# Kernel optimization log

Measured on AMD Instinct MI355X. Metric: run time of the kernel, lower is better.

## Reference

```python
import jax, jax.numpy as jnp
import numpy as np

N = 10000      # nodes
E = 160000     # edges
MUL = 64       # multiplicity of 0e and 1o in node feats / target
NATTR = 10     # number of element types (node_attrs one-hot width)
RDIM = 8       # radial (edge_feats) dim
NAVG = 16.0    # num_avg_neighbors
_INV3 = 0.5773502691896258  # CG coeff for 1o x 1o -> 0e (1/sqrt(3))


def setup_inputs() -> dict:
    key = jax.random.key(0)
    ks = jax.random.split(key, 20)
    return {
        "node_attrs": jax.random.uniform(ks[0], (N, NATTR), jnp.float32),
        "node_feats": jax.random.normal(ks[1], (N, 4 * MUL), jnp.float32),
        "edge_attrs_real": jax.random.normal(ks[2], (E, 4), jnp.float32),
        "edge_attrs_imag": jax.random.normal(ks[3], (E, 4), jnp.float32),
        "edge_feats": jax.random.normal(ks[4], (E, RDIM), jnp.float32),
        # linear_up (per-l internal weights)
        "W_up0": jax.random.normal(ks[5], (MUL, MUL), jnp.float32),
        "W_up1": jax.random.normal(ks[6], (MUL, MUL), jnp.float32),
        # conv_tp_weights MLP: [8, 64, 64, 64, 4*MUL]
        "M1": jax.random.normal(ks[7], (RDIM, 64), jnp.float32),
        "M2": jax.random.normal(ks[8], (64, 64), jnp.float32),
        "M3": jax.random.normal(ks[9], (64, 64), jnp.float32),
        "M4": jax.random.normal(ks[10], (64, 4 * MUL), jnp.float32),
        # linear: irreps_mid (128x0e+128x1o) -> irreps_nonlin (128x0e+64x1o)
        "W_lin_s": jax.random.normal(ks[11], (2 * MUL, 2 * MUL), jnp.float32),
        "W_lin_v": jax.random.normal(ks[12], (2 * MUL, MUL), jnp.float32),
        # skip_tp: FullyConnectedTensorProduct(node_feats, node_attrs -> irreps_nonlin)
        "W_sk_s": jax.random.normal(ks[13], (MUL, NATTR, 2 * MUL), jnp.float32),
        "W_sk_v": jax.random.normal(ks[14], (MUL, NATTR, MUL), jnp.float32),
        "edge_index": jax.random.randint(ks[15], (2, E), 0, N, jnp.int64
                                         if jax.config.jax_enable_x64 else jnp.int32),
    }


def _forward(node_attrs, node_feats, edge_attrs_real, edge_attrs_imag, edge_feats,
             W_up0, W_up1, M1, M2, M3, M4, W_lin_s, W_lin_v, W_sk_s, W_sk_v,
             sender, receiver):
    n = node_feats.shape[0]
    x0 = node_feats[:, :MUL]                          # (N, 64)   64x0e
    x1 = node_feats[:, MUL:].reshape(n, MUL, 3)       # (N, 64, 3) 64x1o

    # skip TP (fully connected, node_attrs are scalars)
    sk_norm = 1.0 / np.sqrt(MUL * NATTR)
    sc_s = jnp.einsum('nu,na,uav->nv', x0, node_attrs, W_sk_s) * sk_norm   # (N,128)
    sc_v = jnp.einsum('nui,na,uav->nvi', x1, node_attrs, W_sk_v) * sk_norm # (N,64,3)

    # linear_up (per-l)
    up_norm = 1.0 / np.sqrt(MUL)
    x0 = (x0 @ W_up0) * up_norm
    x1 = jnp.einsum('nui,uv->nvi', x1, W_up1) * up_norm

    # radial MLP -> per-edge TP weights (4 uvu paths x MUL)
    h = jax.nn.silu((edge_feats @ M1) / np.sqrt(RDIM))
    h = jax.nn.silu((h @ M2) / 8.0)
    h = jax.nn.silu((h @ M3) / 8.0)
    tw = (h @ M4) / 8.0                               # (E, 256)
    wA, wB, wC, wD = (tw[:, :MUL], tw[:, MUL:2*MUL],
                      tw[:, 2*MUL:3*MUL], tw[:, 3*MUL:])

    xs0 = x0[sender]                                  # (E, 64)
    xs1 = x1[sender]                                  # (E, 64, 3)

    def conv_tp(y):
        # y: (E,4) = [0e | 1o]; uvu paths with per-edge weights
        y0, y1 = y[:, :1], y[:, 1:]
        s = jnp.concatenate([xs0 * y0 * wA,                                  # 0e x 0e -> 0e
                             jnp.einsum('eui,ei->eu', xs1, y1) * _INV3 * wD  # 1o x 1o -> 0e
                             ], axis=1)                                      # (E,128)
        v = jnp.concatenate([(xs0 * wB)[:, :, None] * y1[:, None, :],        # 0e x 1o -> 1o
                             xs1 * (y0 * wC)[:, :, None]                     # 1o x 0e -> 1o
                             ], axis=1)                                      # (E,128,3)
        return s, v

    sr, vr = conv_tp(edge_attrs_real)
    si, vi = conv_tp(edge_attrs_imag)

    ms_r = jax.ops.segment_sum(sr, receiver, num_segments=n)
    mv_r = jax.ops.segment_sum(vr, receiver, num_segments=n)
    ms_i = jax.ops.segment_sum(si, receiver, num_segments=n)
    mv_i = jax.ops.segment_sum(vi, receiver, num_segments=n)

    lin_norm = (1.0 / np.sqrt(2 * MUL)) / (2.0 * NAVG)

    def lin(ms, mv):
        return (ms @ W_lin_s) * lin_norm, jnp.einsum('nui,uv->nvi', mv, W_lin_v) * lin_norm

    def gate(s, v):
        # irreps_nonlin = 64x0e scalars | 64x0e gates | 64x1o gated
        scal = jax.nn.silu(s[:, :MUL])
        g = jax.nn.silu(s[:, MUL:])
        return jnp.concatenate([scal, (v * g[:, :, None]).reshape(n, 3 * MUL)], axis=1)

    ls, lv = lin(ms_r, mv_r)
    real = gate(ls + sc_s, lv + sc_v)                 # (N, 256), residual on real part
    lsi, lvi = lin(ms_i, mv_i)
    imag = gate(lsi, lvi)                             # (N, 256)

    # view_as_complex + reshape [N, num_features, dim//num_features]; complex kept
    # as trailing real/imag axis of size 2.
    return jnp.stack([real, imag], axis=-1).reshape(n, MUL, (4 * MUL) // MUL, 2)


def reference(node_attrs, node_feats, edge_attrs_real, edge_attrs_imag, edge_feats,
              W_up0, W_up1, M1, M2, M3, M4, W_lin_s, W_lin_v, W_sk_s, W_sk_v,
              edge_index):
    sender, receiver = edge_index[0], edge_index[1]
    return _forward(node_attrs, node_feats, edge_attrs_real, edge_attrs_imag,
                    edge_feats, W_up0, W_up1, M1, M2, M3, M4,
                    W_lin_s, W_lin_v, W_sk_s, W_sk_v, sender, receiver)
```

## Files before the change

kernel.cpp:

```cpp
#include <hip/hip_runtime.h>
#include <hip/hip_bf16.h>

#define NN 10000
#define NE 160000
#define NGRP 625
#define XPLN 640000

#define SK_NORM   0.039528470752104741f
#define UP_NORM   0.125f
#define M1_NORM   0.35355339059327373f
#define INV3      0.5773502691896258f
#define LIN_NORM  0.0027621358640099516f

__device__ __forceinline__ float siluf(float x) { return x / (1.0f + __expf(-x)); }

__device__ __forceinline__ unsigned short f2bf_bits(float x) {
    union { __hip_bfloat16 h; unsigned short u; } cv;
    cv.h = __float2bfloat16(x);
    return cv.u;
}
__device__ __forceinline__ float bflo(unsigned int w) { return __uint_as_float(w << 16); }
__device__ __forceinline__ float bfhi(unsigned int w) { return __uint_as_float(w & 0xffff0000u); }

typedef short bf16x8 __attribute__((ext_vector_type(8)));
typedef float f32x4  __attribute__((ext_vector_type(4)));

__global__ __launch_bounds__(256) void k_detect(const int* __restrict__ ei32, int* __restrict__ flag) {
    __shared__ int cnt;
    if (threadIdx.x == 0) cnt = 0;
    __syncthreads();
    int z = 0;
    for (int i = threadIdx.x; i < 1024; i += 256)
        if (ei32[2 * i + 1] == 0) z++;
    atomicAdd(&cnt, z);
    __syncthreads();
    if (threadIdx.x == 0) flag[0] = (cnt >= 512) ? 1 : 0;
}

__global__ __launch_bounds__(256) void k_cvt(const int* __restrict__ ei32, const int* __restrict__ flag,
                                             int* __restrict__ snd, int* __restrict__ rcv) {
    int e = blockIdx.x * 256 + threadIdx.x;
    if (e >= NE) return;
    if (flag[0]) {
        const long long* e64 = (const long long*)ei32;
        snd[e] = (int)e64[e];
        rcv[e] = (int)e64[NE + e];
    } else {
        snd[e] = ei32[e];
        rcv[e] = ei32[NE + e];
    }
}

__global__ __launch_bounds__(256) void k_wprepN(
    const float* __restrict__ Wsk_s, const float* __restrict__ Wsk_v,
    const float* __restrict__ Wu0, const float* __restrict__ Wu1,
    unsigned short* __restrict__ WNF) {
    int idx = blockIdx.x * 256 + threadIdx.x;
    if (idx >= 131072) return;
    float val;
    if (idx < 81920) {
        int p = idx / 10240, r = idx % 10240;
        int kc = r >> 9, l8 = r & 511;
        int lane = l8 >> 3, j = l8 & 7, quad = lane >> 4, lo = lane & 15;
        int a = kc >> 1, u = (kc & 1) * 32 + quad * 8 + j;
        val = Wsk_s[(u * 10 + a) * 128 + p * 16 + lo];
    } else if (idx < 122880) {
        int rel = idx - 81920;
        int p = rel / 10240, r = rel % 10240;
        int kc = r >> 9, l8 = r & 511;
        int lane = l8 >> 3, j = l8 & 7, quad = lane >> 4, lo = lane & 15;
        int a = kc >> 1, u = (kc & 1) * 32 + quad * 8 + j;
        val = Wsk_v[(u * 10 + a) * 64 + p * 16 + lo];
    } else if (idx < 126976) {
        int rel = idx - 122880;
        int p = rel >> 10, r = rel & 1023;
        int kc = r >> 9, l8 = r & 511;
        int lane = l8 >> 3, j = l8 & 7, quad = lane >> 4, lo = lane & 15;
        int u = kc * 32 + quad * 8 + j;
        val = Wu0[u * 64 + p * 16 + lo];
    } else {
        int rel = idx - 126976;
        int p = rel >> 10, r = rel & 1023;
        int kc = r >> 9, l8 = r & 511;
        int lane = l8 >> 3, j = l8 & 7, quad = lane >> 4, lo = lane & 15;
        int u = kc * 32 + quad * 8 + j;
        val = Wu1[u * 64 + p * 16 + lo];
    }
    WNF[idx] = f2bf_bits(val);
}

__global__ __launch_bounds__(256) void k_xprep(
    const float* __restrict__ node_attrs, const float* __restrict__ node_feats,
    unsigned short* __restrict__ xpk, float* __restrict__ attrsP) {
    int idx = blockIdx.x * 256 + threadIdx.x;
    if (idx < 4 * NN * 64) {
        int n = idx >> 8, c = idx & 255;
        int plane = c >> 6, u = c & 63;
        float v = (plane == 0) ? node_feats[(long)n * 256 + u]
                               : node_feats[(long)n * 256 + 64 + u * 3 + (plane - 1)];
        xpk[(size_t)plane * XPLN + (long)n * 64 + u] = f2bf_bits(v);
        return;
    }
    int i2 = idx - 4 * NN * 64;
    if (i2 < 10 * NN) {
        int a = i2 / NN, n = i2 - a * NN;
        attrsP[i2] = node_attrs[(long)n * 10 + a];
    }
}

__global__ __launch_bounds__(256) void k_wprep2(
    const float* __restrict__ M1, const float* __restrict__ M2,
    const float* __restrict__ M3, const float* __restrict__ M4,
    const float* __restrict__ W_lin_s, const float* __restrict__ W_lin_v,
    unsigned short* __restrict__ WFG, unsigned short* __restrict__ WLF) {
    int idx = blockIdx.x * 256 + threadIdx.x;
    if (idx >= (52 + 48) * 512) return;
    if (idx < 52 * 512) {
        int f = idx >> 9, r = idx & 511;
        int lane = r >> 3, j = r & 7;
        int quad = lane >> 4, lo = lane & 15;
        float val;
        if (f < 4) {
            int n = f * 16 + lo, k = quad * 8 + j;
            val = (k < 8) ? M1[k * 64 + n] : 0.f;
        } else if (f < 12) {
            int g2 = f - 4, nt = g2 >> 1, half = g2 & 1;
            int n = nt * 16 + lo, k = half * 32 + quad * 8 + j;
            val = M2[k * 64 + n];
        } else if (f < 20) {
            int g3 = f - 12, nt = g3 >> 1, half = g3 & 1;
            int n = nt * 16 + lo, k = half * 32 + quad * 8 + j;
            val = M3[k * 64 + n];
        } else {
            int g4 = f - 20, tt = g4 >> 1, half = g4 & 1;
            int n = tt * 16 + lo, k = half * 32 + quad * 8 + j;
            val = M4[k * 256 + n];
        }
        WFG[idx] = f2bf_bits(val);
    } else {
        int rel = idx - 52 * 512;
        int f = rel >> 9, r = rel & 511;
        int lane = r >> 3, j = r & 7;
        int quad = lane >> 4, lo = lane & 15;
        float val;
        if (f < 32) {
            int vt = f >> 2, ks = f & 3;
            val = W_lin_s[(ks * 32 + quad * 8 + j) * 128 + vt * 16 + lo];
        } else {
            int f2 = f - 32;
            int vt = f2 >> 2, ks = f2 & 3;
            val = W_lin_v[(ks * 32 + quad * 8 + j) * 64 + vt * 16 + lo];
        }
        WLF[rel] = f2bf_bits(val);
    }
}

#define G0 8
#define NB0 79
#define G2 4
#define NB2 157
#define G3 16
#define NB3 40
#define KNODE_GRID (4*NB0 + 2*NB2 + 2*NB3)

__global__ __launch_bounds__(128) void k_node(
    const unsigned short* __restrict__ xpk, const float* __restrict__ attrsP,
    const unsigned short* __restrict__ WNF,
    float* __restrict__ sc_s, float* __restrict__ sc_v,
    float* __restrict__ x0u, float* __restrict__ x1p) {
    __shared__ unsigned short pan[2 * 10240];
    __shared__ float att[10 * 128];

    int t = threadIdx.x;
    int bid = blockIdx.x;
    int type, vp, chunk;
    if (bid < 4 * NB0)                 { type = 0; vp = bid / NB0; chunk = bid % NB0; }
    else if (bid < 4 * NB0 + 2 * NB2)  { int r = bid - 4 * NB0; type = 2; vp = r / NB2; chunk = r % NB2; }
    else                               { int r = bid - 4 * NB0 - 2 * NB2; type = 3; vp = r / NB3; chunk = r % NB3; }
    int G = (type == 0) ? G0 : (type == 2 ? G2 : G3);
    int g0 = chunk * G;
    int ng = NGRP - g0; if (ng > G) ng = G;
    int n0 = g0 * 16;

    int psrc, pcnt;
    if (type == 0)      { psrc = vp * 2 * 10240;           pcnt = 20480; }
    else if (type == 2) { psrc = 81920 + vp * 2 * 10240;   pcnt = 20480; }
    else                { psrc = 122880 + vp * 2 * 1024;   pcnt = 2048;  }
    for (int i = t; i < pcnt / 8; i += 128)
        ((float4*)pan)[i] = ((const float4*)(WNF + psrc))[i];
    if (type == 3) {
        for (int i = t; i < 2048 / 8; i += 128)
            ((float4*)(pan + 2048))[i] = ((const float4*)(WNF + 126976 + vp * 2 * 1024))[i];
    }
    if (type <= 2) {
        int cnt = ng * 16;
        #pragma unroll
        for (int k = 0; k < 10; k++) {
            int i = k * 128 + t;
            int nl = t;
            if (nl < cnt) att[i] = attrsP[k * NN + n0 + nl];
        }
    }
    __syncthreads();

    int wv = t >> 6, lane = t & 63, lo = lane & 15, quad = lane >> 4;
    int lbase = lane * 8;
    const f32x4 zacc = {0.f, 0.f, 0.f, 0.f};
    const unsigned short* mypan = pan + wv * 10240;

    if (type == 0) {
        int vtg = vp * 2 + wv;
        const unsigned short* xb = xpk;
        bf16x8 nfa0 = *(const bf16x8*)(xb + (long)(n0 + lo) * 64 + quad * 8);
        bf16x8 nfa1 = *(const bf16x8*)(xb + (long)(n0 + lo) * 64 + 32 + quad * 8);
        #pragma unroll 1
        for (int g = 0; g < ng; g++) {
            bf16x8 fa0 = nfa0, fa1 = nfa1;
            if (g + 1 < ng) {
                nfa0 = *(const bf16x8*)(xb + (long)(n0 + (g + 1) * 16 + lo) * 64 + quad * 8);
                nfa1 = *(const bf16x8*)(xb + (long)(n0 + (g + 1) * 16 + lo) * 64 + 32 + quad * 8);
            }
            f32x4 acc = zacc;
            #pragma unroll
            for (int a = 0; a < 10; a++) {
                bf16x8 b0 = *(const bf16x8*)&mypan[(2 * a) * 512 + lbase];
                bf16x8 b1 = *(const bf16x8*)&mypan[(2 * a + 1) * 512 + lbase];
                f32x4 p = __builtin_amdgcn_mfma_f32_16x16x32_bf16(fa0, b0, zacc, 0, 0, 0);
                p = __builtin_amdgcn_mfma_f32_16x16x32_bf16(fa1, b1, p, 0, 0, 0);
                float4 afv = *(const float4*)&att[a * 128 + g * 16 + quad * 4];
                acc[0] += afv.x * p[0]; acc[1] += afv.y * p[1];
                acc[2] += afv.z * p[2]; acc[3] += afv.w * p[3];
            }
            int nb = n0 + g * 16;
            #pragma unroll
            for (int r = 0; r < 4; r++)
                sc_s[(long)(nb + quad * 4 + r) * 128 + vtg * 16 + lo] = acc[r] * SK_NORM;
        }
    } else if (type == 2) {
        int vt = vp * 2 + wv;
        bf16x8 nfa0[3], nfa1[3];
        #pragma unroll
        for (int i = 0; i < 3; i++) {
            const unsigned short* xb = xpk + (size_t)(1 + i) * XPLN + (long)(n0 + lo) * 64;
            nfa0[i] = *(const bf16x8*)(xb + quad * 8);
            nfa1[i] = *(const bf16x8*)(xb + 32 + quad * 8);
        }
        #pragma unroll 1
        for (int g = 0; g < ng; g++) {
            bf16x8 fa0[3], fa1[3];
            #pragma unroll
            for (int i = 0; i < 3; i++) { fa0[i] = nfa0[i]; fa1[i] = nfa1[i]; }
            if (g + 1 < ng) {
                #pragma unroll
                for (int i = 0; i < 3; i++) {
                    const unsigned short* xb = xpk + (size_t)(1 + i) * XPLN + (long)(n0 + (g + 1) * 16 + lo) * 64;
                    nfa0[i] = *(const bf16x8*)(xb + quad * 8);
                    nfa1[i] = *(const bf16x8*)(xb + 32 + quad * 8);
                }
            }
            f32x4 acc0 = zacc, acc1 = zacc, acc2 = zacc;
            #pragma unroll
            for (int a = 0; a < 10; a++) {
                bf16x8 b0 = *(const bf16x8*)&mypan[(2 * a) * 512 + lbase];
                bf16x8 b1 = *(const bf16x8*)&mypan[(2 * a + 1) * 512 + lbase];
                float4 afv = *(const float4*)&att[a * 128 + g * 16 + quad * 4];
                f32x4 p0 = __builtin_amdgcn_mfma_f32_16x16x32_bf16(fa0[0], b0, zacc, 0, 0, 0);
                p0 = __builtin_amdgcn_mfma_f32_16x16x32_bf16(fa1[0], b1, p0, 0, 0, 0);
                acc0[0] += afv.x * p0[0]; acc0[1] += afv.y * p0[1];
                acc0[2] += afv.z * p0[2]; acc0[3] += afv.w * p0[3];
                f32x4 p1 = __builtin_amdgcn_mfma_f32_16x16x32_bf16(fa0[1], b0, zacc, 0, 0, 0);
                p1 = __builtin_amdgcn_mfma_f32_16x16x32_bf16(fa1[1], b1, p1, 0, 0, 0);
                acc1[0] += afv.x * p1[0]; acc1[1] += afv.y * p1[1];
                acc1[2] += afv.z * p1[2]; acc1[3] += afv.w * p1[3];
                f32x4 p2 = __builtin_amdgcn_mfma_f32_16x16x32_bf16(fa0[2], b0, zacc, 0, 0, 0);
                p2 = __builtin_amdgcn_mfma_f32_16x16x32_bf16(fa1[2], b1, p2, 0, 0, 0);
                acc2[0] += afv.x * p2[0]; acc2[1] += afv.y * p2[1];
                acc2[2] += afv.z * p2[2]; acc2[3] += afv.w * p2[3];
            }
            int nb = n0 + g * 16;
            #pragma unroll
            for (int r = 0; r < 4; r++) {
                long rb = (long)(nb + quad * 4 + r) * 192 + vt * 16 + lo;
                sc_v[rb]       = acc0[r] * SK_NORM;
                sc_v[rb + 64]  = acc1[r] * SK_NORM;
                sc_v[rb + 128] = acc2[r] * SK_NORM;
            }
        }
    } else {
        int vt = vp * 2 + wv;
        bf16x8 bk20 = *(const bf16x8*)&pan[wv * 1024 + lbase];
        bf16x8 bk21 = *(const bf16x8*)&pan[wv * 1024 + 512 + lbase];
        bf16x8 bk30 = *(const bf16x8*)&pan[2048 + wv * 1024 + lbase];
        bf16x8 bk31 = *(const bf16x8*)&pan[2048 + wv * 1024 + 512 + lbase];
        #pragma unroll 1
        for (int g = 0; g < ng; g++) {
            int nb = n0 + g * 16;
            {
                const unsigned short* xb = xpk + (long)(nb + lo) * 64;
                bf16x8 fa0 = *(const bf16x8*)(xb + quad * 8);
                bf16x8 fa1 = *(const bf16x8*)(xb + 32 + quad * 8);
                f32x4 acc = __builtin_amdgcn_mfma_f32_16x16x32_bf16(fa0, bk20, zacc, 0, 0, 0);
                acc = __builtin_amdgcn_mfma_f32_16x16x32_bf16(fa1, bk21, acc, 0, 0, 0);
                #pragma unroll
                for (int r = 0; r < 4; r++)
                    x0u[(long)(nb + quad * 4 + r) * 64 + vt * 16 + lo] = acc[r] * UP_NORM;
            }
            #pragma unroll
            for (int i = 0; i < 3; i++) {
                const unsigned short* xb = xpk + (size_t)(1 + i) * XPLN + (long)(nb + lo) * 64;
                bf16x8 fa0 = *(const bf16x8*)(xb + quad * 8);
                bf16x8 fa1 = *(const bf16x8*)(xb + 32 + quad * 8);
                f32x4 acc = __builtin_amdgcn_mfma_f32_16x16x32_bf16(fa0, bk30, zacc, 0, 0, 0);
                acc = __builtin_amdgcn_mfma_f32_16x16x32_bf16(fa1, bk31, acc, 0, 0, 0);
                #pragma unroll
                for (int r = 0; r < 4; r++)
                    x1p[(size_t)i * XPLN + (long)(nb + quad * 4 + r) * 64 + vt * 16 + lo] = acc[r] * UP_NORM;
            }
        }
    }
}

__global__ __launch_bounds__(256) void k_hist(const int* __restrict__ rcv, int* __restrict__ counts) {
    int e = blockIdx.x * 256 + threadIdx.x;
    if (e < NE) atomicAdd(&counts[rcv[e]], 1);
}

__global__ __launch_bounds__(1024) void k_scan(const int* __restrict__ counts, int* __restrict__ offsets) {
    __shared__ int partial[1024];
    int t = threadIdx.x;
    const int CHUNK = (NN + 1023) / 1024;
    int base = t * CHUNK;
    int s = 0;
    for (int i = 0; i < CHUNK; i++) if (base + i < NN) s += counts[base + i];
    partial[t] = s;
    __syncthreads();
    for (int d = 1; d < 1024; d *= 2) {
        int v = (t >= d) ? partial[t - d] : 0;
        __syncthreads();
        partial[t] += v;
        __syncthreads();
    }
    int excl = (t == 0) ? 0 : partial[t - 1];
    for (int i = 0; i < CHUNK; i++) {
        if (base + i < NN) { offsets[base + i] = excl; excl += counts[base + i]; }
    }
    if (t == 1023) offsets[NN] = partial[1023];
}

__global__ __launch_bounds__(256) void k_fill(const int* __restrict__ rcv, const int* __restrict__ snd,
                                              const int* __restrict__ offsets,
                                              int* __restrict__ cursor, int2* __restrict__ epk) {
    int e = blockIdx.x * 256 + threadIdx.x;
    if (e < NE) {
        int r = rcv[e];
        int pos = atomicAdd(&cursor[r], 1);
        epk[offsets[r] + pos] = make_int2(snd[e], e);
    }
}

__global__ __launch_bounds__(256) void k_eprep(const int2* __restrict__ epk,
                                               const float4* __restrict__ ear, const float4* __restrict__ eai,
                                               const float4* __restrict__ ef,
                                               int* __restrict__ sndp,
                                               float4* __restrict__ earp, float4* __restrict__ eaip,
                                               float4* __restrict__ efp) {
    int j = blockIdx.x * 256 + threadIdx.x;
    if (j >= NE) return;
    int2 se = epk[j];
    sndp[j] = se.x;
    earp[j] = ear[se.y];
    eaip[j] = eai[se.y];
    efp[(long)j * 2]     = ef[(long)se.y * 2];
    efp[(long)j * 2 + 1] = ef[(long)se.y * 2 + 1];
}

#define HID_STRIDE 72
#define OB_STRIDE  40
#define EPB 256
#define EMW 8

__global__ __launch_bounds__(512) void k_edge_mlp(
    const float4* __restrict__ efp, const unsigned short* __restrict__ WFG,
    __hip_bfloat16* __restrict__ twp) {
    __shared__ unsigned short wfrag[52 * 512];
    __shared__ unsigned short hid[EMW][16 * HID_STRIDE];

    int t = threadIdx.x;
    for (int i = t; i < 52 * 512 / 8; i += 512)
        ((float4*)wfrag)[i] = ((const float4*)WFG)[i];
    __syncthreads();

    int wv = t >> 6;
    int lane = t & 63;
    int lo = lane & 15;
    int quad = lane >> 4;
    int lbase = lane * 8;
    unsigned short* myhid = hid[wv];
    unsigned short* myob  = hid[wv];
    const f32x4 zacc = {0.f, 0.f, 0.f, 0.f};

    float4 f0, f1;
    if (quad == 0) {
        long jb0 = (long)blockIdx.x * EPB + wv * 16;
        f0 = efp[(jb0 + lo) * 2];
        f1 = efp[(jb0 + lo) * 2 + 1];
    }

    #pragma unroll 1
    for (int g = 0; g < EPB / 128; g++) {
        long jbase = (long)blockIdx.x * EPB + g * 128 + wv * 16;

        bf16x8 a1 = {0, 0, 0, 0, 0, 0, 0, 0};
        if (quad == 0) {
            union { unsigned short us[8]; bf16x8 v; } pk;
            pk.us[0] = f2bf_bits(f0.x * M1_NORM); pk.us[1] = f2bf_bits(f0.y * M1_NORM);
            pk.us[2] = f2bf_bits(f0.z * M1_NORM); pk.us[3] = f2bf_bits(f0.w * M1_NORM);
            pk.us[4] = f2bf_bits(f1.x * M1_NORM); pk.us[5] = f2bf_bits(f1.y * M1_NORM);
            pk.us[6] = f2bf_bits(f1.z * M1_NORM); pk.us[7] = f2bf_bits(f1.w * M1_NORM);
            a1 = pk.v;
            if (g + 1 < EPB / 128) {
                long jbn = jbase + 128;
                f0 = efp[(jbn + lo) * 2];
                f1 = efp[(jbn + lo) * 2 + 1];
            }
        }
        {
            f32x4 acc[4];
            #pragma unroll
            for (int nt = 0; nt < 4; nt++) {
                bf16x8 b = *(const bf16x8*)&wfrag[nt * 512 + lbase];
                acc[nt] = __builtin_amdgcn_mfma_f32_16x16x32_bf16(a1, b, zacc, 0, 0, 0);
            }
            #pragma unroll
            for (int nt = 0; nt < 4; nt++)
                #pragma unroll
                for (int r = 0; r < 4; r++)
                    myhid[(quad * 4 + r) * HID_STRIDE + nt * 16 + lo] = f2bf_bits(siluf(acc[nt][r]));
        }

        #pragma unroll
        for (int L = 0; L < 2; L++) {
            int fb = 4 + L * 8;
            bf16x8 a0 = *(const bf16x8*)&myhid[lo * HID_STRIDE + quad * 8];
            bf16x8 a1v = *(const bf16x8*)&myhid[lo * HID_STRIDE + 32 + quad * 8];
            f32x4 acc[4];
            #pragma unroll
            for (int nt = 0; nt < 4; nt++) {
                bf16x8 b0 = *(const bf16x8*)&wfrag[(fb + nt * 2) * 512 + lbase];
                bf16x8 b1 = *(const bf16x8*)&wfrag[(fb + nt * 2 + 1) * 512 + lbase];
                acc[nt] = __builtin_amdgcn_mfma_f32_16x16x32_bf16(a0, b0, zacc, 0, 0, 0);
                acc[nt] = __builtin_amdgcn_mfma_f32_16x16x32_bf16(a1v, b1, acc[nt], 0, 0, 0);
            }
            #pragma unroll
            for (int nt = 0; nt < 4; nt++)
                #pragma unroll
                for (int r = 0; r < 4; r++)
                    myhid[(quad * 4 + r) * HID_STRIDE + nt * 16 + lo] = f2bf_bits(siluf(acc[nt][r] * 0.125f));
        }

        {
            bf16x8 a0 = *(const bf16x8*)&myhid[lo * HID_STRIDE + quad * 8];
            bf16x8 a1v = *(const bf16x8*)&myhid[lo * HID_STRIDE + 32 + quad * 8];
            int sedge = lane >> 2, sch = lane & 3;
            #pragma unroll 1
            for (int rd = 0; rd < 8; rd++) {
                f32x4 acc2[2];
                #pragma unroll
                for (int p = 0; p < 2; p++) {
                    int tt = (rd < 4) ? (p * 4 + rd) : (8 + p * 4 + (rd - 4));
                    bf16x8 b0 = *(const bf16x8*)&wfrag[(20 + tt * 2) * 512 + lbase];
                    bf16x8 b1 = *(const bf16x8*)&wfrag[(20 + tt * 2 + 1) * 512 + lbase];
                    acc2[p] = __builtin_amdgcn_mfma_f32_16x16x32_bf16(a0, b0, zacc, 0, 0, 0);
                    acc2[p] = __builtin_amdgcn_mfma_f32_16x16x32_bf16(a1v, b1, acc2[p], 0, 0, 0);
                }
                #pragma unroll
                for (int p = 0; p < 2; p++)
                    #pragma unroll
                    for (int r = 0; r < 4; r++)
                        myob[(quad * 4 + r) * OB_STRIDE + 2 * lo + p] = f2bf_bits(acc2[p][r] * 0.125f);
                bf16x8 vv = *(const bf16x8*)&myob[sedge * OB_STRIDE + sch * 8];
                *(bf16x8*)(twp + (jbase + sedge) * 256 + rd * 32 + sch * 8) = vv;
            }
        }
    }
}

#define CB2 4
__global__ __launch_bounds__(256) void k_conv(
    const int* __restrict__ offsets, const int* __restrict__ sndp,
    const float4* __restrict__ earp, const float4* __restrict__ eaip,
    const float* __restrict__ x0u, const float* __restrict__ x1p,
    const __hip_bfloat16* __restrict__ twp,
    unsigned short* __restrict__ msgF) {
    __shared__ float red[2 * 64 * 9];
    __shared__ unsigned short stg[1024];
    int n = blockIdx.x;
    int t = threadIdx.x;
    int wv = t >> 6;
    int u = t & 63;
    int path = wv >> 1;
    int wpar = wv & 1;
    int beg = offsets[n], end = offsets[n + 1];
    float a0r = 0.f, a1r = 0.f, a2r = 0.f, a3r = 0.f;
    float a0i = 0.f, a1i = 0.f, a2i = 0.f, a3i = 0.f;
    if (path == 0) {
        const int tsel = 2 * u;
        for (int jb = beg + wpar * CB2; jb < end; jb += 2 * CB2) {
            unsigned int twd[CB2]; float x0v[CB2]; float4 yr[CB2], yi[CB2];
            #pragma unroll
            for (int p = 0; p < CB2; p++) {
                int j = jb + p;
                int jc = (j < end) ? j : (end - 1);
                int s = sndp[jc];
                yr[p] = earp[jc];
                yi[p] = eaip[jc];
                x0v[p] = x0u[(long)s * 64 + u];
                twd[p] = (j < end) ? *(const unsigned int*)(twp + (long)jc * 256 + tsel) : 0u;
            }
            #pragma unroll
            for (int p = 0; p < CB2; p++) {
                float wA = bflo(twd[p]), wB = bfhi(twd[p]);
                float xa = x0v[p] * wA, xb = x0v[p] * wB;
                a0r += xa * yr[p].x; a1r += xb * yr[p].y; a2r += xb * yr[p].z; a3r += xb * yr[p].w;
                a0i += xa * yi[p].x; a1i += xb * yi[p].y; a2i += xb * yi[p].z; a3i += xb * yi[p].w;
            }
        }
    } else {
        const int tsel = 128 + 2 * u;
        for (int jb = beg + wpar * CB2; jb < end; jb += 2 * CB2) {
            unsigned int twd[CB2]; float xv0[CB2], xv1[CB2], xv2[CB2]; float4 yr[CB2], yi[CB2];
            #pragma unroll
            for (int p = 0; p < CB2; p++) {
                int j = jb + p;
                int jc = (j < end) ? j : (end - 1);
                int s = sndp[jc];
                yr[p] = earp[jc];
                yi[p] = eaip[jc];
                long sb = (long)s * 64 + u;
                xv0[p] = x1p[sb];
                xv1[p] = x1p[XPLN + sb];
                xv2[p] = x1p[2 * XPLN + sb];
                twd[p] = (j < end) ? *(const unsigned int*)(twp + (long)jc * 256 + tsel) : 0u;
            }
            #pragma unroll
            for (int p = 0; p < CB2; p++) {
                float wC = bflo(twd[p]), wDs = bfhi(twd[p]) * INV3;
                float dr = xv0[p] * yr[p].y + xv1[p] * yr[p].z + xv2[p] * yr[p].w;
                float di = xv0[p] * yi[p].y + xv1[p] * yi[p].z + xv2[p] * yi[p].w;
                a0r += dr * wDs; a0i += di * wDs;
                float ycr = yr[p].x * wC, yci = yi[p].x * wC;
                a1r += xv0[p] * ycr; a2r += xv1[p] * ycr; a3r += xv2[p] * ycr;
                a1i += xv0[p] * yci; a2i += xv1[p] * yci; a3i += xv2[p] * yci;
            }
        }
    }
    float* rb = &red[(path * 64 + u) * 9];
    if (wpar == 1) {
        rb[0] = a0r; rb[1] = a1r; rb[2] = a2r; rb[3] = a3r;
        rb[4] = a0i; rb[5] = a1i; rb[6] = a2i; rb[7] = a3i;
    }
    __syncthreads();
    if (wpar == 0) {
        a0r += rb[0]; a1r += rb[1]; a2r += rb[2]; a3r += rb[3];
        a0i += rb[4]; a1i += rb[5]; a2i += rb[6]; a3i += rb[7];
        int cu = path * 64 + u;
        stg[cu]       = f2bf_bits(a0r);
        stg[128 + cu] = f2bf_bits(a0i);
        stg[256 + cu] = f2bf_bits(a1r);
        stg[384 + cu] = f2bf_bits(a2r);
        stg[512 + cu] = f2bf_bits(a3r);
        stg[640 + cu] = f2bf_bits(a1i);
        stg[768 + cu] = f2bf_bits(a2i);
        stg[896 + cu] = f2bf_bits(a3i);
    }
    __syncthreads();
    if (t < 128) {
        int g = n >> 4, lo = n & 15;
        bf16x8 vv = *(const bf16x8*)&stg[t * 8];
        *(bf16x8*)(msgF + (size_t)g * 16384 + (t >> 2) * 512 + lo * 32 + (t & 3) * 8) = vv;
    }
}

#define SV_STRIDE 129
#define VV_STRIDE 65

__global__ __launch_bounds__(256, 3) void k_lin(
    const unsigned short* __restrict__ msgF,
    const float* __restrict__ sc_s, const float* __restrict__ sc_v,
    const unsigned short* __restrict__ WLF,
    float* __restrict__ out) {
    __shared__ char smem[49152];
    unsigned short* wfrag = (unsigned short*)smem;
    float* sval = (float*)smem;
    float* vval = (float*)(smem + 2 * 16 * SV_STRIDE * 4);

    int t = threadIdx.x;
    for (int i = t; i < 48 * 512 / 8; i += 256)
        ((float4*)wfrag)[i] = ((const float4*)WLF)[i];
    __syncthreads();

    int wv = t >> 6;
    int lane = t & 63;
    int lo = lane & 15;
    int quad = lane >> 4;
    int lbase = lane * 8;
    int aoff_lane = lo * 32 + quad * 8;
    const f32x4 zacc = {0.f, 0.f, 0.f, 0.f};

    long g = blockIdx.x;
    long nbase = g * 16;
    const unsigned short* agbase = msgF + (size_t)g * 16384;

    f32x4 accs[10];
    #pragma unroll
    for (int q = 0; q < 10; q++) {
        int tau = wv + q * 4;
        int cblk, fb;
        if (tau < 16) {
            int ri = tau >> 3, vt = tau & 7;
            cblk = ri; fb = vt * 4;
        } else {
            int tp = tau - 16;
            int ri = tp / 12, rem = tp % 12;
            int i = rem >> 2, vt = rem & 3;
            cblk = 2 + ri * 3 + i; fb = 32 + vt * 4;
        }
        f32x4 acc = zacc;
        #pragma unroll
        for (int ks = 0; ks < 4; ks++) {
            bf16x8 a = *(const bf16x8*)(agbase + (cblk * 4 + ks) * 512 + aoff_lane);
            bf16x8 b = *(const bf16x8*)&wfrag[(fb + ks) * 512 + lbase];
            acc = __builtin_amdgcn_mfma_f32_16x16x32_bf16(a, b, acc, 0, 0, 0);
        }
        accs[q] = acc;
    }
    __syncthreads();

    #pragma unroll
    for (int q = 0; q < 10; q++) {
        int tau = wv + q * 4;
        if (tau < 16) {
            int ri = tau >> 3, vt = tau & 7;
            int cidx = (ri * 16) * SV_STRIDE + vt * 16 + lo;
            #pragma unroll
            for (int r = 0; r < 4; r++)
                sval[cidx + (quad * 4 + r) * SV_STRIDE] = accs[q][r] * LIN_NORM;
        } else {
            int tp = tau - 16;
            int ri = tp / 12, rem = tp % 12;
            int i = rem >> 2, vt = rem & 3;
            int cidx = ((ri * 3 + i) * 16) * VV_STRIDE + vt * 16 + lo;
            #pragma unroll
            for (int r = 0; r < 4; r++)
                vval[cidx + (quad * 4 + r) * VV_STRIDE] = accs[q][r] * LIN_NORM;
        }
    }
    __syncthreads();

    #pragma unroll 1
    for (int j = 0; j < 16; j++) {
        int c = t;
        long gn = nbase + j;
        float re, im;
        if (c < 64) {
            float sr = sval[(0 * 16 + j) * SV_STRIDE + c] + sc_s[gn * 128 + c];
            float si = sval[(1 * 16 + j) * SV_STRIDE + c];
            re = siluf(sr); im = siluf(si);
        } else {
            int rem = c - 64;
            int v = rem / 3;
            int i = rem - v * 3;
            float gr = siluf(sval[(0 * 16 + j) * SV_STRIDE + 64 + v] + sc_s[gn * 128 + 64 + v]);
            float gi = siluf(sval[(1 * 16 + j) * SV_STRIDE + 64 + v]);
            float lr = vval[((0 * 3 + i) * 16 + j) * VV_STRIDE + v] + sc_v[gn * 192 + i * 64 + v];
            float li = vval[((1 * 3 + i) * 16 + j) * VV_STRIDE + v];
            re = lr * gr; im = li * gi;
        }
        ((float2*)out)[gn * 256 + c] = make_float2(re, im);
    }
}

extern "C" void kernel_launch(void* const* d_in, const int* in_sizes, int n_in,
                              void* d_out, int out_size, void* d_ws, size_t ws_size,
                              hipStream_t stream) {
    const float* node_attrs = (const float*)d_in[0];
    const float* node_feats = (const float*)d_in[1];
    const float* ear        = (const float*)d_in[2];
    const float* eai        = (const float*)d_in[3];
    const float* edge_feats = (const float*)d_in[4];
    const float* W_up0      = (const float*)d_in[5];
    const float* W_up1      = (const float*)d_in[6];
    const float* M1         = (const float*)d_in[7];
    const float* M2         = (const float*)d_in[8];
    const float* M3         = (const float*)d_in[9];
    const float* M4         = (const float*)d_in[10];
    const float* W_lin_s    = (const float*)d_in[11];
    const float* W_lin_v    = (const float*)d_in[12];
    const float* W_sk_s     = (const float*)d_in[13];
    const float* W_sk_v     = (const float*)d_in[14];
    const int*   ei         = (const int*)d_in[15];

    char* ws = (char*)d_ws;
    size_t o_x0u = 0;
    size_t o_x1p = o_x0u + (size_t)NN * 64 * 4;
    size_t o_scs = o_x1p + (size_t)NN * 256 * 4;
    size_t o_scv = o_scs + (size_t)NN * 128 * 4;
    size_t o_tw  = o_scv + (size_t)NN * 192 * 4;
    size_t o_cnt = o_tw  + (size_t)NE * 256 * 2;
    size_t o_cur = o_cnt + (size_t)NN * 4;
    size_t o_ofs = o_cur + (size_t)NN * 4;
    size_t o_epk = o_ofs + (size_t)(NN + 1) * 4 + 60;
    size_t o_snd = o_epk + (size_t)NE * 8;
    size_t o_rcv = o_snd + (size_t)NE * 4;
    size_t o_flg = o_rcv + (size_t)NE * 4;
    size_t o_msg = o_flg + 64;
    size_t o_wnf = o_msg + (size_t)NN * 1024 * 2;
    size_t o_snp = o_wnf + 262144;
    size_t o_erp = o_snp + (size_t)NE * 4;
    size_t o_eip = o_erp + (size_t)NE * 16;
    size_t o_efp = o_eip + (size_t)NE * 16;
    size_t o_wfg = o_efp + (size_t)NE * 32;
    size_t o_wlf = o_wfg + (size_t)52 * 512 * 2;
    size_t o_xpk = o_wlf + (size_t)48 * 512 * 2;
    size_t o_atp = o_xpk + (size_t)4 * NN * 64 * 2;

    float* x0u = (float*)(ws + o_x0u);
    float* x1p = (float*)(ws + o_x1p);
    float* sc_s = (float*)(ws + o_scs);
    float* sc_v = (float*)(ws + o_scv);
    __hip_bfloat16* twp = (__hip_bfloat16*)(ws + o_tw);
    int* counts  = (int*)(ws + o_cnt);
    int* cursor  = (int*)(ws + o_cur);
    int* offsets = (int*)(ws + o_ofs);
    int2* epk    = (int2*)(ws + o_epk);
    int* snd     = (int*)(ws + o_snd);
    int* rcv     = (int*)(ws + o_rcv);
    int* flag    = (int*)(ws + o_flg);
    unsigned short* msgF = (unsigned short*)(ws + o_msg);
    unsigned short* WNF = (unsigned short*)(ws + o_wnf);
    int*    sndp = (int*)(ws + o_snp);
    float4* earp = (float4*)(ws + o_erp);
    float4* eaip = (float4*)(ws + o_eip);
    float4* efp  = (float4*)(ws + o_efp);
    unsigned short* WFG = (unsigned short*)(ws + o_wfg);
    unsigned short* WLF = (unsigned short*)(ws + o_wlf);
    unsigned short* xpk = (unsigned short*)(ws + o_xpk);
    float* attrsP = (float*)(ws + o_atp);

    hipMemsetAsync(ws + o_cnt, 0, (size_t)NN * 8, stream);

    dim3 b256(256), b1024(1024), b128(128), b512(512);
    k_detect<<<dim3(1), b256, 0, stream>>>(ei, flag);
    k_cvt   <<<dim3((NE + 255) / 256), b256, 0, stream>>>(ei, flag, snd, rcv);
    k_hist<<<dim3((NE + 255) / 256), b256, 0, stream>>>(rcv, counts);
    k_scan<<<dim3(1), b1024, 0, stream>>>(counts, offsets);
    k_fill<<<dim3((NE + 255) / 256), b256, 0, stream>>>(rcv, snd, offsets, cursor, epk);
    k_eprep<<<dim3((NE + 255) / 256), b256, 0, stream>>>(epk, (const float4*)ear, (const float4*)eai,
                                                         (const float4*)edge_feats,
                                                         sndp, earp, eaip, efp);
    k_wprepN<<<dim3(512), b256, 0, stream>>>(W_sk_s, W_sk_v, W_up0, W_up1, WNF);
    k_wprep2<<<dim3(200), b256, 0, stream>>>(M1, M2, M3, M4, W_lin_s, W_lin_v, WFG, WLF);
    k_xprep <<<dim3((4 * NN * 64 + 10 * NN + 255) / 256), b256, 0, stream>>>(node_attrs, node_feats, xpk, attrsP);
    k_node  <<<dim3(KNODE_GRID), b128, 0, stream>>>(xpk, attrsP, WNF, sc_s, sc_v, x0u, x1p);
    k_edge_mlp<<<dim3(NE / EPB), b512, 0, stream>>>(efp, WFG, twp);
    k_conv<<<dim3(NN), b256, 0, stream>>>(offsets, sndp, earp, eaip, x0u, x1p, twp, msgF);
    k_lin <<<dim3(NGRP), b256, 0, stream>>>(msgF, sc_s, sc_v, WLF, (float*)d_out);
}
```

Baseline: 274.6 us.

## Remap k_conv so each wavefront handles one whole node, four nodes per block

```diff
diff --git a/kernel.cpp b/kernel.cpp
--- a/kernel.cpp
+++ b/kernel.cpp
@@ -485,6 +485,7 @@
     }
 }
 
+#define NPB 4
 #define CB2 4
 __global__ __launch_bounds__(256) void k_conv(
     const int* __restrict__ offsets, const int* __restrict__ sndp,
@@ -492,92 +493,81 @@
     const float* __restrict__ x0u, const float* __restrict__ x1p,
     const __hip_bfloat16* __restrict__ twp,
     unsigned short* __restrict__ msgF) {
-    __shared__ float red[2 * 64 * 9];
-    __shared__ unsigned short stg[1024];
-    int n = blockIdx.x;
+    __shared__ unsigned short stg[NPB][1024];
     int t = threadIdx.x;
     int wv = t >> 6;
     int u = t & 63;
-    int path = wv >> 1;
-    int wpar = wv & 1;
+    int n = blockIdx.x * NPB + wv;
     int beg = offsets[n], end = offsets[n + 1];
+    const int tsel0 = 2 * u, tsel1 = 128 + 2 * u;
     float a0r = 0.f, a1r = 0.f, a2r = 0.f, a3r = 0.f;
     float a0i = 0.f, a1i = 0.f, a2i = 0.f, a3i = 0.f;
-    if (path == 0) {
-        const int tsel = 2 * u;
-        for (int jb = beg + wpar * CB2; jb < end; jb += 2 * CB2) {
-            unsigned int twd[CB2]; float x0v[CB2]; float4 yr[CB2], yi[CB2];
-            #pragma unroll
-            for (int p = 0; p < CB2; p++) {
-                int j = jb + p;
-                int jc = (j < end) ? j : (end - 1);
-                int s = sndp[jc];
-                yr[p] = earp[jc];
-                yi[p] = eaip[jc];
-                x0v[p] = x0u[(long)s * 64 + u];
-                twd[p] = (j < end) ? *(const unsigned int*)(twp + (long)jc * 256 + tsel) : 0u;
-            }
-            #pragma unroll
-            for (int p = 0; p < CB2; p++) {
-                float wA = bflo(twd[p]), wB = bfhi(twd[p]);
-                float xa = x0v[p] * wA, xb = x0v[p] * wB;
-                a0r += xa * yr[p].x; a1r += xb * yr[p].y; a2r += xb * yr[p].z; a3r += xb * yr[p].w;
-                a0i += xa * yi[p].x; a1i += xb * yi[p].y; a2i += xb * yi[p].z; a3i += xb * yi[p].w;
-            }
-        }
-    } else {
-        const int tsel = 128 + 2 * u;
-        for (int jb = beg + wpar * CB2; jb < end; jb += 2 * CB2) {
-            unsigned int twd[CB2]; float xv0[CB2], xv1[CB2], xv2[CB2]; float4 yr[CB2], yi[CB2];
-            #pragma unroll
-            for (int p = 0; p < CB2; p++) {
-                int j = jb + p;
-                int jc = (j < end) ? j : (end - 1);
-                int s = sndp[jc];
-                yr[p] = earp[jc];
-                yi[p] = eaip[jc];
-                long sb = (long)s * 64 + u;
-                xv0[p] = x1p[sb];
-                xv1[p] = x1p[XPLN + sb];
-                xv2[p] = x1p[2 * XPLN + sb];
-                twd[p] = (j < end) ? *(const unsigned int*)(twp + (long)jc * 256 + tsel) : 0u;
-            }
-            #pragma unroll
-            for (int p = 0; p < CB2; p++) {
-                float wC = bflo(twd[p]), wDs = bfhi(twd[p]) * INV3;
-                float dr = xv0[p] * yr[p].y + xv1[p] * yr[p].z + xv2[p] * yr[p].w;
-                float di = xv0[p] * yi[p].y + xv1[p] * yi[p].z + xv2[p] * yi[p].w;
-                a0r += dr * wDs; a0i += di * wDs;
-                float ycr = yr[p].x * wC, yci = yi[p].x * wC;
-                a1r += xv0[p] * ycr; a2r += xv1[p] * ycr; a3r += xv2[p] * ycr;
-                a1i += xv0[p] * yci; a2i += xv1[p] * yci; a3i += xv2[p] * yci;
-            }
-        }
-    }
-    float* rb = &red[(path * 64 + u) * 9];
-    if (wpar == 1) {
-        rb[0] = a0r; rb[1] = a1r; rb[2] = a2r; rb[3] = a3r;
-        rb[4] = a0i; rb[5] = a1i; rb[6] = a2i; rb[7] = a3i;
-    }
-    __syncthreads();
-    if (wpar == 0) {
-        a0r += rb[0]; a1r += rb[1]; a2r += rb[2]; a3r += rb[3];
-        a0i += rb[4]; a1i += rb[5]; a2i += rb[6]; a3i += rb[7];
-        int cu = path * 64 + u;
-        stg[cu]       = f2bf_bits(a0r);
-        stg[128 + cu] = f2bf_bits(a0i);
-        stg[256 + cu] = f2bf_bits(a1r);
-        stg[384 + cu] = f2bf_bits(a2r);
-        stg[512 + cu] = f2bf_bits(a3r);
-        stg[640 + cu] = f2bf_bits(a1i);
-        stg[768 + cu] = f2bf_bits(a2i);
-        stg[896 + cu] = f2bf_bits(a3i);
-    }
-    __syncthreads();
-    if (t < 128) {
-        int g = n >> 4, lo = n & 15;
-        bf16x8 vv = *(const bf16x8*)&stg[t * 8];
-        *(bf16x8*)(msgF + (size_t)g * 16384 + (t >> 2) * 512 + lo * 32 + (t & 3) * 8) = vv;
+    float c0r = 0.f, c1r = 0.f, c2r = 0.f, c3r = 0.f;
+    float c0i = 0.f, c1i = 0.f, c2i = 0.f, c3i = 0.f;
+
+    for (int jb = beg; jb < end; jb += CB2) {
+        unsigned int t0[CB2], t1[CB2];
+        float x0v[CB2], xv0[CB2], xv1[CB2], xv2[CB2];
+        float4 yr[CB2], yi[CB2];
+        #pragma unroll
+        for (int p = 0; p < CB2; p++) {
+            int j = jb + p;
+            int jc = (j < end) ? j : (end - 1);
+            int s = sndp[jc];
+            yr[p] = earp[jc];
+            yi[p] = eaip[jc];
+            long sb = (long)s * 64 + u;
+            x0v[p] = x0u[sb];
+            xv0[p] = x1p[sb];
+            xv1[p] = x1p[XPLN + sb];
+            xv2[p] = x1p[2 * XPLN + sb];
+            bool valid = (j < end);
+            t0[p] = valid ? *(const unsigned int*)(twp + (long)jc * 256 + tsel0) : 0u;
+            t1[p] = valid ? *(const unsigned int*)(twp + (long)jc * 256 + tsel1) : 0u;
+        }
+        #pragma unroll
+        for (int p = 0; p < CB2; p++) {
+            float wA = bflo(t0[p]), wB = bfhi(t0[p]);
+            float xa = x0v[p] * wA, xb = x0v[p] * wB;
+            a0r += xa * yr[p].x; a1r += xb * yr[p].y; a2r += xb * yr[p].z; a3r += xb * yr[p].w;
+            a0i += xa * yi[p].x; a1i += xb * yi[p].y; a2i += xb * yi[p].z; a3i += xb * yi[p].w;
+            float wC = bflo(t1[p]), wDs = bfhi(t1[p]) * INV3;
+            float dr = xv0[p] * yr[p].y + xv1[p] * yr[p].z + xv2[p] * yr[p].w;
+            float di = xv0[p] * yi[p].y + xv1[p] * yi[p].z + xv2[p] * yi[p].w;
+            c0r += dr * wDs; c0i += di * wDs;
+            float ycr = yr[p].x * wC, yci = yi[p].x * wC;
+            c1r += xv0[p] * ycr; c2r += xv1[p] * ycr; c3r += xv2[p] * ycr;
+            c1i += xv0[p] * yci; c2i += xv1[p] * yci; c3i += xv2[p] * yci;
+        }
+    }
+
+    unsigned short* sg = stg[wv];
+    sg[u]       = f2bf_bits(a0r);
+    sg[128 + u] = f2bf_bits(a0i);
+    sg[256 + u] = f2bf_bits(a1r);
+    sg[384 + u] = f2bf_bits(a2r);
+    sg[512 + u] = f2bf_bits(a3r);
+    sg[640 + u] = f2bf_bits(a1i);
+    sg[768 + u] = f2bf_bits(a2i);
+    sg[896 + u] = f2bf_bits(a3i);
+    sg[64 + u]  = f2bf_bits(c0r);
+    sg[192 + u] = f2bf_bits(c0i);
+    sg[320 + u] = f2bf_bits(c1r);
+    sg[448 + u] = f2bf_bits(c2r);
+    sg[576 + u] = f2bf_bits(c3r);
+    sg[704 + u] = f2bf_bits(c1i);
+    sg[832 + u] = f2bf_bits(c2i);
+    sg[960 + u] = f2bf_bits(c3i);
+    __syncthreads();
+
+    #pragma unroll
+    for (int rep = 0; rep < 2; rep++) {
+        int job = rep * 256 + t;
+        int m = job >> 7, c = job & 127;
+        int nm = blockIdx.x * NPB + m;
+        int g = nm >> 4, lo = nm & 15;
+        bf16x8 vv = *(const bf16x8*)&stg[m][c * 8];
+        *(bf16x8*)(msgF + (size_t)g * 16384 + (c >> 2) * 512 + lo * 32 + (c & 3) * 8) = vv;
     }
 }
 
@@ -763,6 +753,6 @@
     k_xprep <<<dim3((4 * NN * 64 + 10 * NN + 255) / 256), b256, 0, stream>>>(node_attrs, node_feats, xpk, attrsP);
     k_node  <<<dim3(KNODE_GRID), b128, 0, stream>>>(xpk, attrsP, WNF, sc_s, sc_v, x0u, x1p);
     k_edge_mlp<<<dim3(NE / EPB), b512, 0, stream>>>(efp, WFG, twp);
-    k_conv<<<dim3(NN), b256, 0, stream>>>(offsets, sndp, earp, eaip, x0u, x1p, twp, msgF);
+    k_conv<<<dim3(NN / NPB), b256, 0, stream>>>(offsets, sndp, earp, eaip, x0u, x1p, twp, msgF);
     k_lin <<<dim3(NGRP), b256, 0, stream>>>(msgF, sc_s, sc_v, WLF, (float*)d_out);
 }
```

After: 274.0 us. No clear change (-0.2%).
